# Optimization experiments

Measured on AMD Instinct MI355X. Metric: run time of the kernel, lower is better.

## Reference

```python
import jax, jax.numpy as jnp
import numpy as np

B, L, D = 32, 256, 1024
ALIGN = 1024
FF = 2048
NUM_CLASSES = 3


def setup_inputs() -> dict:
    key = jax.random.key(0)
    ks = jax.random.split(key, 10)
    u = lambda k, shape: jax.random.uniform(k, shape, jnp.float32, -1.0, 1.0)
    return {
        "premises": jax.random.normal(ks[0], (B, L, D), jnp.float32),
        "hypotheses": jax.random.normal(ks[1], (B, L, D), jnp.float32),
        "W_F": u(ks[2], (D, ALIGN)),
        "W_G": u(ks[3], (2 * D, FF)),
        "W1": u(ks[4], (2 * FF, FF)) * 0.02,
        "b1": jnp.zeros((FF,), jnp.float32),
        "W2": u(ks[5], (FF, FF)) * 0.02,
        "b2": jnp.zeros((FF,), jnp.float32),
        "W3": u(ks[6], (FF, NUM_CLASSES)) * 0.02,
        "b3": jnp.zeros((NUM_CLASSES,), jnp.float32),
    }


def reference(premises, hypotheses, W_F, W_G, W1, b1, W2, b2, W3, b3):
    # ---- align: tanh-projected cross attention ----
    F_p = jnp.tanh(jnp.einsum("bpd,da->bpa", premises, W_F))      # [B,Lp,A]
    F_h = jnp.tanh(jnp.einsum("bhd,da->bha", hypotheses, W_F))    # [B,Lh,A]
    eijs = jnp.einsum("bpa,bha->bph", F_p, F_h)                   # [B,Lp,Lh]
    attn = jax.nn.softmax(eijs, axis=-1)                          # tf.nn.softmax: last axis
    betas = jnp.einsum("bph,bhd->bpd", attn, hypotheses)          # [B,Lp,D]
    alphas = jnp.einsum("bph,bpd->bhd", attn, premises)           # [B,Lh,D]

    # ---- compare (dropout is identity: p_keep = 1.0 at eval) ----
    V1 = jnp.tanh(jnp.concatenate([premises, betas], axis=2) @ W_G)    # [B,Lp,FF]
    V2 = jnp.tanh(jnp.concatenate([hypotheses, alphas], axis=2) @ W_G) # [B,Lh,FF]

    # ---- aggregate: sum-pool over sequence, concat ----
    agg = jnp.concatenate([V1.sum(axis=1), V2.sum(axis=1)], axis=1)    # [B,2*FF]

    # ---- classifier MLP ----
    a1 = jnp.tanh(agg @ W1 + b1)
    a2 = jnp.tanh(a1 @ W2 + b2)
    logits = a2 @ W3 + b3                                              # [B,3]
    return logits
```

## Files before the change

### kernel.cpp

```cpp
#include <hip/hip_runtime.h>
#include <hip/hip_bf16.h>
#include <stdint.h>


typedef __attribute__((ext_vector_type(8))) short    short8_t;
typedef __attribute__((ext_vector_type(4))) float    float4_t;
typedef __attribute__((ext_vector_type(8))) _Float16 half8_t;
typedef __attribute__((ext_vector_type(4))) _Float16 half4_t;
typedef __attribute__((ext_vector_type(2))) _Float16 half2_t;

#define DEVI static __device__ __forceinline__

DEVI short f2bf(float f) {
  union { float f; unsigned u; } v; v.f = f;
  unsigned r = v.u + 0x7fffu + ((v.u >> 16) & 1u);
  return (short)(r >> 16);
}
DEVI float bf2f(short s) {
  union { unsigned u; float f; } v;
  v.u = ((unsigned)(unsigned short)s) << 16;
  return v.f;
}
DEVI void split2(float x, short& hi, short& lo) {
  hi = f2bf(x);
  lo = f2bf(x - bf2f(hi));
}
DEVI float fast_tanh(float x) {
  float e = __expf(2.0f * x);
  return 1.0f - 2.0f / (e + 1.0f);
}
DEVI void gload16(const void* g, void* l) {
  __builtin_amdgcn_global_load_lds(
      (const __attribute__((address_space(1))) void*)g,
      (__attribute__((address_space(3))) void*)l, 16, 0, 0);
}

template <int DO_TANH, int OUT_MODE>
__global__ __launch_bounds__(256) void gemm_nt_split(
    const short* __restrict__ Ah, const short* __restrict__ Al, int lda, long sA,
    const short* __restrict__ Bh, const short* __restrict__ Bl, int ldb, long sB,
    void* __restrict__ Ch, void* __restrict__ Cl, int ldc, long sC,
    int M, int K, int kslices)
{
  __shared__ __align__(16) short Ash[128 * 32];
  __shared__ __align__(16) short Asl[128 * 32];
  __shared__ __align__(16) short Bsh[128 * 32];
  __shared__ __align__(16) short Bsl[128 * 32];

  const int z  = blockIdx.z;
  const int zb = z / kslices;
  const int zk = z - zb * kslices;
  const int Ksub = K / kslices;
  const int kbeg = zk * Ksub, kend = kbeg + Ksub;

  Ah += (size_t)zb * sA;  Al += (size_t)zb * sA;
  Bh += (size_t)zb * sB;  Bl += (size_t)zb * sB;

  const int row0 = blockIdx.x * 128;
  const int col0 = blockIdx.y * 128;

  const int t    = threadIdx.x;
  const int lane = t & 63;
  const int wave = t >> 6;
  const int wr = wave >> 1, wc = wave & 1;
  const int m15 = lane & 15, q = lane >> 4;

  const int schk = ((t & 3) ^ ((t >> 3) & 3)) * 8;
  const short* pAh = Ah + (size_t)(row0 + (t >> 2)) * lda + kbeg + schk;
  const short* pAl = Al + (size_t)(row0 + (t >> 2)) * lda + kbeg + schk;
  const short* pBh = Bh + (size_t)(col0 + (t >> 2)) * ldb + kbeg + schk;
  const short* pBl = Bl + (size_t)(col0 + (t >> 2)) * ldb + kbeg + schk;
  const size_t a64 = (size_t)64 * lda, b64 = (size_t)64 * ldb;
  short* lAh = &Ash[wave * 512];
  short* lAl = &Asl[wave * 512];
  short* lBh = &Bsh[wave * 512];
  short* lBl = &Bsl[wave * 512];

  const int fs2 = (q ^ ((m15 >> 1) & 3)) * 8;

  float4_t acc[4][4];
#pragma unroll
  for (int i = 0; i < 4; ++i)
#pragma unroll
    for (int j = 0; j < 4; ++j) acc[i][j] = (float4_t)0.0f;

  for (int k0 = kbeg; k0 < kend; k0 += 32) {
    gload16(pAh, lAh);  gload16(pAh + a64, lAh + 2048);
    gload16(pAl, lAl);  gload16(pAl + a64, lAl + 2048);
    gload16(pBh, lBh);  gload16(pBh + b64, lBh + 2048);
    gload16(pBl, lBl);  gload16(pBl + b64, lBl + 2048);
    pAh += 32; pAl += 32; pBh += 32; pBl += 32;
    __syncthreads();

    short8_t ah[4], al[4];
#pragma unroll
    for (int i = 0; i < 4; ++i) {
      const int ra = (wr * 64 + i * 16 + m15) * 32 + fs2;
      ah[i] = *(const short8_t*)&Ash[ra];
      al[i] = *(const short8_t*)&Asl[ra];
    }
#pragma unroll
    for (int j = 0; j < 4; ++j) {
      const int rb = (wc * 64 + j * 16 + m15) * 32 + fs2;
      short8_t bh = *(const short8_t*)&Bsh[rb];
      short8_t bl = *(const short8_t*)&Bsl[rb];
#pragma unroll
      for (int i = 0; i < 4; ++i) {
        acc[i][j] = __builtin_amdgcn_mfma_f32_16x16x32_bf16(ah[i], bh, acc[i][j], 0, 0, 0);
        acc[i][j] = __builtin_amdgcn_mfma_f32_16x16x32_bf16(ah[i], bl, acc[i][j], 0, 0, 0);
        acc[i][j] = __builtin_amdgcn_mfma_f32_16x16x32_bf16(al[i], bh, acc[i][j], 0, 0, 0);
      }
    }
    __syncthreads();
  }

  short* Chs = (short*)Ch + (size_t)zb * sC;
  short* Cls = (short*)Cl + (size_t)zb * sC;
  float* Cf  = (float*)Ch + (size_t)zb * sC;
#pragma unroll
  for (int i = 0; i < 4; ++i) {
#pragma unroll
    for (int r = 0; r < 4; ++r) {
      int gm = row0 + wr * 64 + i * 16 + q * 4 + r;
      if (gm < M) {
#pragma unroll
        for (int j = 0; j < 4; ++j) {
          int gn = col0 + wc * 64 + j * 16 + m15;
          float v = acc[i][j][r];
          if (DO_TANH) v = fast_tanh(v);
          if (OUT_MODE == 0) {
            atomicAdd(&Cf[(size_t)gm * ldc + gn], v);
          } else {
            short hi, lo; split2(v, hi, lo);
            Chs[(size_t)gm * ldc + gn] = hi;
            Cls[(size_t)gm * ldc + gn] = lo;
          }
        }
      }
    }
  }
}

__global__ __launch_bounds__(256) void gemm_f16(
    const _Float16* __restrict__ A, int lda, long sA,
    const _Float16* __restrict__ B, int ldb, long sB,
    _Float16* __restrict__ C, int ldc, long sC,
    int K, int bxor)
{
  __shared__ __align__(16) _Float16 As[2 * 128 * 32];
  __shared__ __align__(16) _Float16 Bs[2 * 128 * 32];

  const int z = blockIdx.z;
  A += (size_t)z * sA;
  B += (size_t)(z ^ bxor) * sB;

  const int row0 = blockIdx.x * 128;
  const int col0 = blockIdx.y * 128;
  const int t = threadIdx.x, lane = t & 63, wave = t >> 6;
  const int wr = wave >> 1, wc = wave & 1;
  const int m15 = lane & 15, q = lane >> 4;

  const int srow = wave * 32 + (lane >> 2);
  const int cg   = ((lane & 3) ^ ((lane >> 3) & 3)) * 8;
  const _Float16* gA0 = A + (size_t)(row0 + srow) * lda + cg;
  const _Float16* gA1 = gA0 + (size_t)16 * lda;
  const _Float16* gB0 = B + (size_t)(col0 + srow) * ldb + cg;
  const _Float16* gB1 = gB0 + (size_t)16 * ldb;
  const _Float16* gA0b = gA0 + 32;
  const _Float16* gA1b = gA1 + 32;
  const _Float16* gB0b = gB0 + 32;
  const _Float16* gB1b = gB1 + 32;
  _Float16* lA0  = &As[(wave * 32) * 32];
  _Float16* lA1  = &As[(wave * 32 + 16) * 32];
  _Float16* lB0  = &Bs[(wave * 32) * 32];
  _Float16* lB1  = &Bs[(wave * 32 + 16) * 32];
  _Float16* lA0b = lA0 + 4096;
  _Float16* lA1b = lA1 + 4096;
  _Float16* lB0b = lB0 + 4096;
  _Float16* lB1b = lB1 + 4096;

  const int fs = (q ^ ((m15 >> 1) & 3)) * 8;
  int aoff[4], boff[4];
#pragma unroll
  for (int i = 0; i < 4; ++i) {
    aoff[i] = (wr * 64 + i * 16 + m15) * 32 + fs;
    boff[i] = (wc * 64 + i * 16 + m15) * 32 + fs;
  }

  float4_t acc[4][4];
#pragma unroll
  for (int i = 0; i < 4; ++i)
#pragma unroll
    for (int j = 0; j < 4; ++j) acc[i][j] = (float4_t)0.0f;

  for (int k0 = 0; k0 < K; k0 += 64) {
    gload16(gA0, lA0);  gload16(gA1, lA1);
    gload16(gB0, lB0);  gload16(gB1, lB1);
    gload16(gA0b, lA0b); gload16(gA1b, lA1b);
    gload16(gB0b, lB0b); gload16(gB1b, lB1b);
    gA0 += 64; gA1 += 64; gB0 += 64; gB1 += 64;
    gA0b += 64; gA1b += 64; gB0b += 64; gB1b += 64;
    __syncthreads();

#pragma unroll
    for (int h = 0; h < 2; ++h) {
      half8_t af[4], bfr[4];
#pragma unroll
      for (int i = 0; i < 4; ++i) af[i]  = *(const half8_t*)&As[h * 4096 + aoff[i]];
#pragma unroll
      for (int j = 0; j < 4; ++j) bfr[j] = *(const half8_t*)&Bs[h * 4096 + boff[j]];
#pragma unroll
      for (int i = 0; i < 4; ++i)
#pragma unroll
        for (int j = 0; j < 4; ++j)
          acc[i][j] = __builtin_amdgcn_mfma_f32_16x16x32_f16(af[i], bfr[j], acc[i][j], 0, 0, 0);
    }
    __syncthreads();
  }

  {
    _Float16* Cp = C + (size_t)z * sC;
#pragma unroll
    for (int i = 0; i < 4; ++i)
#pragma unroll
      for (int r = 0; r < 4; ++r) {
        int gm = row0 + wr * 64 + i * 16 + q * 4 + r;
#pragma unroll
        for (int j = 0; j < 4; ++j) {
          int gn = col0 + wc * 64 + j * 16 + m15;
          Cp[(size_t)gm * ldc + gn] = (_Float16)acc[i][j][r];
        }
      }
  }
}

__global__ __launch_bounds__(512, 2) void gemm_f16_sum8(
    const _Float16* __restrict__ A, int lda,
    const _Float16* __restrict__ B, int ldb,
    int K, float* __restrict__ agg)
{
  __shared__ __align__(16) _Float16 LDS[4][2 * 256 * 32];

  const int row0 = blockIdx.x * 256;
  const int col0 = blockIdx.y * 256;
  const int tid  = threadIdx.x;
  const int lane = tid & 63, wave = tid >> 6;
  const int wr = wave >> 2, wc = wave & 3;
  const int m15 = lane & 15, q = lane >> 4;
  const int nt = K / 32;

  const int srow = wave * 32 + (lane >> 2);
  const int cg   = ((lane & 3) ^ ((lane >> 3) & 3)) * 8;
  const _Float16* gA = A + (size_t)(row0 + srow) * lda + cg;
  const _Float16* gB = B + (size_t)(col0 + srow) * ldb + cg;

  auto stageA = [&](int t) {
    const _Float16* g = gA + t * 32;
    _Float16* l = &LDS[t & 3][wave * 1024];
    gload16(g, l);
    gload16(g + (size_t)16 * lda, l + 512);
  };
  auto stageB = [&](int t) {
    const _Float16* g = gB + t * 32;
    _Float16* l = &LDS[t & 3][8192 + wave * 1024];
    gload16(g, l);
    gload16(g + (size_t)16 * ldb, l + 512);
  };

  const int xq = (q ^ ((m15 >> 1) & 3)) * 8;
  int aoff[8], boff[4];
#pragma unroll
  for (int i = 0; i < 8; ++i)
    aoff[i] = (wr * 128 + i * 16 + m15) * 32 + xq;
#pragma unroll
  for (int j = 0; j < 4; ++j)
    boff[j] = 8192 + (wc * 64 + j * 16 + m15) * 32 + xq;

  float4_t acc[8][4];
#pragma unroll
  for (int i = 0; i < 8; ++i)
#pragma unroll
    for (int j = 0; j < 4; ++j) acc[i][j] = (float4_t)0.0f;

  stageA(0); stageB(0);
  stageA(1); stageB(1);
  asm volatile("s_waitcnt vmcnt(4)");
  __builtin_amdgcn_s_barrier();

  for (int t = 0; t < nt; ++t) {
    const _Float16* buf = &LDS[t & 3][0];
    __builtin_amdgcn_sched_barrier(0);

    half8_t a0[4], a1[4], bb[4];
#pragma unroll
    for (int i = 0; i < 4; ++i) a0[i] = *(const half8_t*)&buf[aoff[i]];
#pragma unroll
    for (int j = 0; j < 4; ++j) bb[j] = *(const half8_t*)&buf[boff[j]];
#pragma unroll
    for (int i = 0; i < 4; ++i) a1[i] = *(const half8_t*)&buf[aoff[4 + i]];

    if (t + 2 < nt) { stageA(t + 2); stageB(t + 2); }

    __builtin_amdgcn_s_setprio(1);
#pragma unroll
    for (int i = 0; i < 4; ++i)
#pragma unroll
      for (int j = 0; j < 4; ++j)
        acc[i][j] = __builtin_amdgcn_mfma_f32_16x16x32_f16(a0[i], bb[j], acc[i][j], 0, 0, 0);
#pragma unroll
    for (int i = 0; i < 4; ++i)
#pragma unroll
      for (int j = 0; j < 4; ++j)
        acc[4 + i][j] = __builtin_amdgcn_mfma_f32_16x16x32_f16(a1[i], bb[j], acc[4 + i][j], 0, 0, 0);
    __builtin_amdgcn_s_setprio(0);

    __builtin_amdgcn_sched_barrier(0);
    if (t + 2 < nt) {
      asm volatile("s_waitcnt vmcnt(4)");
    } else if (t + 1 < nt) {
      asm volatile("s_waitcnt vmcnt(0)");
    }
    __builtin_amdgcn_s_barrier();
  }

  const int half_ = row0 >= 8192;
  const int b     = (row0 & 8191) >> 8;
#pragma unroll
  for (int j = 0; j < 4; ++j) {
    float s = 0.0f;
#pragma unroll
    for (int i = 0; i < 8; ++i)
#pragma unroll
      for (int r = 0; r < 4; ++r) s += fast_tanh(acc[i][j][r]);
    s += __shfl_xor(s, 16);
    s += __shfl_xor(s, 32);
    if (q == 0) {
      int col = col0 + wc * 64 + j * 16 + m15;
      atomicAdd(&agg[(size_t)b * 4096 + half_ * 2048 + col], s);
    }
  }
}

__global__ __launch_bounds__(256) void transpose_split(
    const float* __restrict__ in, short* __restrict__ oh, short* __restrict__ ol,
    int R, int C)
{
  __shared__ float tile[32][33];
  const int tx = threadIdx.x & 31, ty = threadIdx.x >> 5;
  const int c0 = blockIdx.x * 32, r0 = blockIdx.y * 32;
#pragma unroll
  for (int i = 0; i < 4; ++i) {
    int r = ty + i * 8;
    tile[r][tx] = in[(size_t)(r0 + r) * C + c0 + tx];
  }
  __syncthreads();
#pragma unroll
  for (int i = 0; i < 4; ++i) {
    int cc = ty + i * 8;
    float v = tile[tx][cc];
    short hi, lo; split2(v, hi, lo);
    size_t o = (size_t)(c0 + cc) * R + r0 + tx;
    oh[o] = hi;
    ol[o] = lo;
  }
}

__global__ __launch_bounds__(256) void transpose_f16(
    const float* __restrict__ in, _Float16* __restrict__ out, int R, int C)
{
  __shared__ float tile[32][33];
  const int tx = threadIdx.x & 31, ty = threadIdx.x >> 5;
  const int c0 = blockIdx.x * 32, r0 = blockIdx.y * 32;
#pragma unroll
  for (int i = 0; i < 4; ++i) {
    int r = ty + i * 8;
    tile[r][tx] = in[(size_t)(r0 + r) * C + c0 + tx];
  }
  __syncthreads();
#pragma unroll
  for (int i = 0; i < 4; ++i) {
    int cc = ty + i * 8;
    out[(size_t)(c0 + cc) * R + r0 + tx] = (_Float16)tile[tx][cc];
  }
}

__global__ __launch_bounds__(256) void transpose_b2b(
    const short* __restrict__ in, short* __restrict__ out,
    int R, int C, long sIn, long sOut)
{
  __shared__ short tile[32][33];
  in  += (size_t)blockIdx.z * sIn;
  out += (size_t)blockIdx.z * sOut;
  const int tx = threadIdx.x & 31, ty = threadIdx.x >> 5;
  const int c0 = blockIdx.x * 32, r0 = blockIdx.y * 32;
#pragma unroll
  for (int i = 0; i < 4; ++i) {
    int r = ty + i * 8;
    tile[r][tx] = in[(size_t)(r0 + r) * C + c0 + tx];
  }
  __syncthreads();
#pragma unroll
  for (int i = 0; i < 4; ++i) {
    int cc = ty + i * 8;
    out[(size_t)(c0 + cc) * R + r0 + tx] = tile[tx][cc];
  }
}

__global__ __launch_bounds__(256) void conv_in_t(
    const float* __restrict__ P, const float* __restrict__ Hh,
    short* __restrict__ oh, short* __restrict__ ol,
    _Float16* __restrict__ cat, _Float16* __restrict__ phbt)
{
  __shared__ __align__(16) float tile[64][68];
  const int zb   = blockIdx.z;
  const int half = zb >> 5, b = zb & 31;
  const float* in = (half ? Hh : P) + (size_t)b * 256 * 1024;
  const int c0 = blockIdx.x * 64;
  const int r0 = blockIdx.y * 64;
  const int t  = threadIdx.x;
  const int rl = t >> 4;
  const int c4 = (t & 15) * 4;
  const size_t rowbase = (size_t)half * 8192 + (size_t)b * 256;
#pragma unroll
  for (int i = 0; i < 4; ++i) {
    int r = rl + i * 16;
    float4 v = *(const float4*)&in[(size_t)(r0 + r) * 1024 + c0 + c4];
    *(float4*)&tile[r][c4] = v;
    short4 h, l;
    split2(v.x, h.x, l.x); split2(v.y, h.y, l.y);
    split2(v.z, h.z, l.z); split2(v.w, h.w, l.w);
    size_t o = (rowbase + r0 + r) * 1024 + c0 + c4;
    *(short4*)&oh[o] = h;
    *(short4*)&ol[o] = l;
    half4_t c16;
    c16.x = (_Float16)v.x; c16.y = (_Float16)v.y;
    c16.z = (_Float16)v.z; c16.w = (_Float16)v.w;
    *(half4_t*)&cat[(rowbase + r0 + r) * 2048 + c0 + c4] = c16;
  }
  __syncthreads();
  _Float16* op = phbt + (size_t)zb * 1024 * 256;
  const int tx = t & 31;
  const int w  = t >> 5;
#pragma unroll
  for (int i = 0; i < 8; ++i) {
    int cc = w + i * 8;
    half2_t p;
    p.x = (_Float16)tile[tx * 2][cc];
    p.y = (_Float16)tile[tx * 2 + 1][cc];
    *(half2_t*)&op[(size_t)(c0 + cc) * 256 + r0 + tx * 2] = p;
  }
}

__global__ __launch_bounds__(256) void zero_f32(float* __restrict__ p, int n)
{
  int i = blockIdx.x * 256 + threadIdx.x;
  if (i < n) p[i] = 0.0f;
}

__global__ __launch_bounds__(256) void softmax_rows(
    const float* __restrict__ e, _Float16* __restrict__ attn)
{
  const int row  = blockIdx.x * 4 + (threadIdx.x >> 6);
  const int lane = threadIdx.x & 63;
  const float4 v = *(const float4*)&e[(size_t)row * 256 + lane * 4];
  float m = fmaxf(fmaxf(v.x, v.y), fmaxf(v.z, v.w));
#pragma unroll
  for (int off = 32; off; off >>= 1) m = fmaxf(m, __shfl_xor(m, off));
  float e0 = __expf(v.x - m), e1 = __expf(v.y - m);
  float e2 = __expf(v.z - m), e3 = __expf(v.w - m);
  float s = e0 + e1 + e2 + e3;
#pragma unroll
  for (int off = 32; off; off >>= 1) s += __shfl_xor(s, off);
  float inv = 1.0f / s;
  half4_t o;
  o.x = (_Float16)(e0 * inv); o.y = (_Float16)(e1 * inv);
  o.z = (_Float16)(e2 * inv); o.w = (_Float16)(e3 * inv);
  *(half4_t*)&attn[(size_t)row * 256 + lane * 4] = o;
}

__global__ __launch_bounds__(256) void skinny_gemm(
    const float* __restrict__ A, const float* __restrict__ B,
    float* __restrict__ out, int N, int K)
{
  __shared__ float Asl[256][33];
  const int n0 = blockIdx.x * 64;
  const int k0 = blockIdx.y * 256;
  const int t  = threadIdx.x;
#pragma unroll
  for (int j = 0; j < 32; ++j) {
    Asl[t][j] = A[(size_t)j * K + k0 + t];
  }
  __syncthreads();
  const int l = t & 63, w = t >> 6;
  const int n = n0 + l;
  float acc[8] = {0.f, 0.f, 0.f, 0.f, 0.f, 0.f, 0.f, 0.f};
  const float* Bp = B + (size_t)k0 * N + n;
#pragma unroll 4
  for (int k = 0; k < 256; ++k) {
    float bv = Bp[(size_t)k * N];
#pragma unroll
    for (int m = 0; m < 8; ++m)
      acc[m] += Asl[k][w * 8 + m] * bv;
  }
#pragma unroll
  for (int m = 0; m < 8; ++m)
    atomicAdd(&out[(size_t)(w * 8 + m) * N + n], acc[m]);
}

__global__ __launch_bounds__(256) void bias_tanh_f32(
    const float* __restrict__ c, const float* __restrict__ bias,
    float* __restrict__ o, int n)
{
  int i = blockIdx.x * 256 + threadIdx.x;
  if (i < n) o[i] = fast_tanh(c[i] + bias[i & 2047]);
}

__global__ __launch_bounds__(256) void logits2(
    const float* __restrict__ c2f, const float* __restrict__ b2,
    const float* __restrict__ W3, const float* __restrict__ b3,
    float* __restrict__ out)
{
  const int b = blockIdx.x, t = threadIdx.x;
  float p0 = 0.f, p1 = 0.f, p2 = 0.f;
  for (int k = t; k < 2048; k += 256) {
    float a = fast_tanh(c2f[b * 2048 + k] + b2[k]);
    p0 += a * W3[k * 3 + 0];
    p1 += a * W3[k * 3 + 1];
    p2 += a * W3[k * 3 + 2];
  }
#pragma unroll
  for (int off = 32; off; off >>= 1) {
    p0 += __shfl_xor(p0, off);
    p1 += __shfl_xor(p1, off);
    p2 += __shfl_xor(p2, off);
  }
  __shared__ float red[4][3];
  if ((t & 63) == 0) {
    red[t >> 6][0] = p0; red[t >> 6][1] = p1; red[t >> 6][2] = p2;
  }
  __syncthreads();
  if (t < 3) out[b * 3 + t] = b3[t] + red[0][t] + red[1][t] + red[2][t] + red[3][t];
}

extern "C" void kernel_launch(void* const* d_in, const int* in_sizes, int n_in,
                              void* d_out, int out_size, void* d_ws, size_t ws_size,
                              hipStream_t stream) {
  (void)in_sizes; (void)n_in; (void)out_size; (void)ws_size;
  const float* P   = (const float*)d_in[0];
  const float* H   = (const float*)d_in[1];
  const float* W_F = (const float*)d_in[2];
  const float* W_G = (const float*)d_in[3];
  const float* W1  = (const float*)d_in[4];
  const float* b1  = (const float*)d_in[5];
  const float* W2  = (const float*)d_in[6];
  const float* b2  = (const float*)d_in[7];
  const float* W3  = (const float*)d_in[8];
  const float* b3  = (const float*)d_in[9];
  float* out = (float*)d_out;

  char* wsp = (char*)d_ws;
  auto alloc = [&](size_t bytes) {
    char* p = wsp;
    wsp += (bytes + 255) & ~(size_t)255;
    return p;
  };
  short*    Pp_h  = (short*)alloc(16384ull * 1024 * 2);
  short*    Pp_l  = (short*)alloc(16384ull * 1024 * 2);
  _Float16* Cat16 = (_Float16*)alloc(16384ull * 2048 * 2);
  short*    Fbuf  = (short*)alloc(32ull * 1024 * 1024 * 2);
  _Float16* PHbT  = (_Float16*)alloc(64ull * 1024 * 256 * 2);
  short*    WFT_h = (short*)alloc(1024ull * 1024 * 2);
  short*    WFT_l = (short*)alloc(1024ull * 1024 * 2);
  _Float16* WGT16 = (_Float16*)alloc(2048ull * 2048 * 2);
  float*    eijs  = (float*)alloc(32ull * 256 * 256 * 4);
  _Float16* attn  = (_Float16*)alloc(32ull * 256 * 256 * 2);
  _Float16* attnT = (_Float16*)alloc(32ull * 256 * 256 * 2);
  float*    agg   = (float*)alloc(32ull * 4096 * 4);
  float*    c1f   = (float*)alloc(32ull * 2048 * 4);
  float*    c2f   = (float*)alloc(32ull * 2048 * 4);
  float*    a1f   = (float*)alloc(32ull * 2048 * 4);

  short* F_h = Fbuf;
  short* F_l = Fbuf + 16384ull * 1024;

  conv_in_t<<<dim3(16, 4, 64), 256, 0, stream>>>(P, H, Pp_h, Pp_l, Cat16, PHbT);
  transpose_split<<<dim3(32, 32, 1), 256, 0, stream>>>(W_F, WFT_h, WFT_l, 1024, 1024);
  transpose_f16<<<dim3(64, 64, 1), 256, 0, stream>>>(W_G, WGT16, 2048, 2048);

  gemm_nt_split<1, 1><<<dim3(128, 8, 1), 256, 0, stream>>>(
      Pp_h, Pp_l, 1024, 0, WFT_h, WFT_l, 1024, 0,
      F_h, F_l, 1024, 0, 16384, 1024, 1);

  zero_f32<<<8192, 256, 0, stream>>>(eijs, 32 * 256 * 256);
  gemm_nt_split<0, 0><<<dim3(2, 2, 128), 256, 0, stream>>>(
      F_h, F_l, 1024, 256 * 1024,
      F_h + 8192ull * 1024, F_l + 8192ull * 1024, 1024, 256 * 1024,
      eijs, nullptr, 256, 65536, 256, 1024, 4);

  softmax_rows<<<2048, 256, 0, stream>>>(eijs, attn);
  transpose_b2b<<<dim3(8, 8, 32), 256, 0, stream>>>(
      (const short*)attn, (short*)attnT, 256, 256, 65536, 65536);

  gemm_f16<<<dim3(2, 8, 64), 256, 0, stream>>>(
      attn, 256, 65536, PHbT, 256, 1024 * 256,
      Cat16 + 1024, 2048, 256 * 2048, 256, 32);

  zero_f32<<<512, 256, 0, stream>>>(agg, 32 * 4096);
  gemm_f16_sum8<<<dim3(64, 8, 1), 512, 0, stream>>>(
      Cat16, 2048, WGT16, 2048, 2048, agg);

  zero_f32<<<256, 256, 0, stream>>>(c1f, 32 * 2048);
  skinny_gemm<<<dim3(32, 16), 256, 0, stream>>>(agg, W1, c1f, 2048, 4096);
  bias_tanh_f32<<<256, 256, 0, stream>>>(c1f, b1, a1f, 32 * 2048);
  zero_f32<<<256, 256, 0, stream>>>(c2f, 32 * 2048);
  skinny_gemm<<<dim3(32, 8), 256, 0, stream>>>(a1f, W2, c2f, 2048, 2048);
  logits2<<<32, 256, 0, stream>>>(c2f, b2, W3, b3, out);
}
```

Baseline: 595.9 us.

## Replace split-K atomics with partial buffers and fuse zeroing and weight transposes

Split-K GEMMs (eijs and both classifier skinny GEMMs) now write per-slice partials into reused scratch buffers instead of atomically adding into zeroed outputs. The consumers (softmax, bias_tanh, logits) sum the slices themselves. This removes the zero_f32 launches and the atomic traffic. The two weight transposes are merged into one launch, and the agg zeroing moves into conv_in_t, cutting kernel launch count in exchange for extra partial-buffer reads.

```diff
diff --git a/kernel.cpp b/kernel.cpp
--- a/kernel.cpp
+++ b/kernel.cpp
@@ -49,8 +49,8 @@
 
   const int z  = blockIdx.z;
   const int zb = z / kslices;
+  const int Ksub = K / kslices;
   const int zk = z - zb * kslices;
-  const int Ksub = K / kslices;
   const int kbeg = zk * Ksub, kend = kbeg + Ksub;
 
   Ah += (size_t)zb * sA;  Al += (size_t)zb * sA;
@@ -116,7 +116,7 @@
 
   short* Chs = (short*)Ch + (size_t)zb * sC;
   short* Cls = (short*)Cl + (size_t)zb * sC;
-  float* Cf  = (float*)Ch + (size_t)zb * sC;
+  float* Cf  = (float*)Ch + (size_t)(OUT_MODE == 2 ? z : zb) * sC;
 #pragma unroll
   for (int i = 0; i < 4; ++i) {
 #pragma unroll
@@ -128,8 +128,8 @@
           int gn = col0 + wc * 64 + j * 16 + m15;
           float v = acc[i][j][r];
           if (DO_TANH) v = fast_tanh(v);
-          if (OUT_MODE == 0) {
-            atomicAdd(&Cf[(size_t)gm * ldc + gn], v);
+          if (OUT_MODE == 2) {
+            Cf[(size_t)gm * ldc + gn] = v;
           } else {
             short hi, lo; split2(v, hi, lo);
             Chs[(size_t)gm * ldc + gn] = hi;
@@ -341,46 +341,44 @@
   }
 }
 
-__global__ __launch_bounds__(256) void transpose_split(
-    const float* __restrict__ in, short* __restrict__ oh, short* __restrict__ ol,
-    int R, int C)
+__global__ __launch_bounds__(256) void transpose_w(
+    const float* __restrict__ WF, short* __restrict__ oh, short* __restrict__ ol,
+    const float* __restrict__ WG, _Float16* __restrict__ og)
 {
   __shared__ float tile[32][33];
+  const int id = blockIdx.x;
   const int tx = threadIdx.x & 31, ty = threadIdx.x >> 5;
-  const int c0 = blockIdx.x * 32, r0 = blockIdx.y * 32;
-#pragma unroll
-  for (int i = 0; i < 4; ++i) {
-    int r = ty + i * 8;
-    tile[r][tx] = in[(size_t)(r0 + r) * C + c0 + tx];
-  }
-  __syncthreads();
-#pragma unroll
-  for (int i = 0; i < 4; ++i) {
-    int cc = ty + i * 8;
-    float v = tile[tx][cc];
-    short hi, lo; split2(v, hi, lo);
-    size_t o = (size_t)(c0 + cc) * R + r0 + tx;
-    oh[o] = hi;
-    ol[o] = lo;
-  }
-}
-
-__global__ __launch_bounds__(256) void transpose_f16(
-    const float* __restrict__ in, _Float16* __restrict__ out, int R, int C)
-{
-  __shared__ float tile[32][33];
-  const int tx = threadIdx.x & 31, ty = threadIdx.x >> 5;
-  const int c0 = blockIdx.x * 32, r0 = blockIdx.y * 32;
-#pragma unroll
-  for (int i = 0; i < 4; ++i) {
-    int r = ty + i * 8;
-    tile[r][tx] = in[(size_t)(r0 + r) * C + c0 + tx];
-  }
-  __syncthreads();
-#pragma unroll
-  for (int i = 0; i < 4; ++i) {
-    int cc = ty + i * 8;
-    out[(size_t)(c0 + cc) * R + r0 + tx] = (_Float16)tile[tx][cc];
+  if (id < 1024) {
+    const int c0 = (id & 31) * 32, r0 = (id >> 5) * 32;
+#pragma unroll
+    for (int i = 0; i < 4; ++i) {
+      int r = ty + i * 8;
+      tile[r][tx] = WF[(size_t)(r0 + r) * 1024 + c0 + tx];
+    }
+    __syncthreads();
+#pragma unroll
+    for (int i = 0; i < 4; ++i) {
+      int cc = ty + i * 8;
+      float v = tile[tx][cc];
+      short hi, lo; split2(v, hi, lo);
+      size_t o = (size_t)(c0 + cc) * 1024 + r0 + tx;
+      oh[o] = hi;
+      ol[o] = lo;
+    }
+  } else {
+    const int t2 = id - 1024;
+    const int c0 = (t2 & 63) * 32, r0 = (t2 >> 6) * 32;
+#pragma unroll
+    for (int i = 0; i < 4; ++i) {
+      int r = ty + i * 8;
+      tile[r][tx] = WG[(size_t)(r0 + r) * 2048 + c0 + tx];
+    }
+    __syncthreads();
+#pragma unroll
+    for (int i = 0; i < 4; ++i) {
+      int cc = ty + i * 8;
+      og[(size_t)(c0 + cc) * 2048 + r0 + tx] = (_Float16)tile[tx][cc];
+    }
   }
 }
 
@@ -409,11 +407,17 @@
 __global__ __launch_bounds__(256) void conv_in_t(
     const float* __restrict__ P, const float* __restrict__ Hh,
     short* __restrict__ oh, short* __restrict__ ol,
-    _Float16* __restrict__ cat, _Float16* __restrict__ phbt)
+    _Float16* __restrict__ cat, _Float16* __restrict__ phbt,
+    float* __restrict__ agg)
 {
   __shared__ __align__(16) float tile[64][68];
   const int zb   = blockIdx.z;
   const int half = zb >> 5, b = zb & 31;
+  const int bid = (zb * 4 + blockIdx.y) * 16 + blockIdx.x;
+  if (bid < 128) {
+    float4_t zz = (float4_t)0.0f;
+    *(float4_t*)&agg[(size_t)bid * 1024 + threadIdx.x * 4] = zz;
+  }
   const float* in = (half ? Hh : P) + (size_t)b * 256 * 1024;
   const int c0 = blockIdx.x * 64;
   const int r0 = blockIdx.y * 64;
@@ -451,18 +455,22 @@
   }
 }
 
-__global__ __launch_bounds__(256) void zero_f32(float* __restrict__ p, int n)
-{
-  int i = blockIdx.x * 256 + threadIdx.x;
-  if (i < n) p[i] = 0.0f;
-}
-
 __global__ __launch_bounds__(256) void softmax_rows(
     const float* __restrict__ e, _Float16* __restrict__ attn)
 {
   const int row  = blockIdx.x * 4 + (threadIdx.x >> 6);
   const int lane = threadIdx.x & 63;
-  const float4 v = *(const float4*)&e[(size_t)row * 256 + lane * 4];
+  const size_t base = ((size_t)(row >> 8) * 4) * 65536
+                    + (size_t)(row & 255) * 256 + lane * 4;
+  const float4 v0 = *(const float4*)&e[base];
+  const float4 v1 = *(const float4*)&e[base + 65536];
+  const float4 v2 = *(const float4*)&e[base + 2 * 65536];
+  const float4 v3 = *(const float4*)&e[base + 3 * 65536];
+  float4 v;
+  v.x = (v0.x + v1.x) + (v2.x + v3.x);
+  v.y = (v0.y + v1.y) + (v2.y + v3.y);
+  v.z = (v0.z + v1.z) + (v2.z + v3.z);
+  v.w = (v0.w + v1.w) + (v2.w + v3.w);
   float m = fmaxf(fmaxf(v.x, v.y), fmaxf(v.z, v.w));
 #pragma unroll
   for (int off = 32; off; off >>= 1) m = fmaxf(m, __shfl_xor(m, off));
@@ -480,7 +488,7 @@
 
 __global__ __launch_bounds__(256) void skinny_gemm(
     const float* __restrict__ A, const float* __restrict__ B,
-    float* __restrict__ out, int N, int K)
+    float* __restrict__ outp, int N, int K)
 {
   __shared__ float Asl[256][33];
   const int n0 = blockIdx.x * 64;
@@ -502,28 +510,36 @@
     for (int m = 0; m < 8; ++m)
       acc[m] += Asl[k][w * 8 + m] * bv;
   }
+  float* o = outp + (size_t)blockIdx.y * 32 * N;
 #pragma unroll
   for (int m = 0; m < 8; ++m)
-    atomicAdd(&out[(size_t)(w * 8 + m) * N + n], acc[m]);
-}
-
-__global__ __launch_bounds__(256) void bias_tanh_f32(
-    const float* __restrict__ c, const float* __restrict__ bias,
-    float* __restrict__ o, int n)
+    o[(size_t)(w * 8 + m) * N + n] = acc[m];
+}
+
+__global__ __launch_bounds__(256) void bias_sum_tanh(
+    const float* __restrict__ parts, int nslice,
+    const float* __restrict__ bias, float* __restrict__ o, int n)
 {
   int i = blockIdx.x * 256 + threadIdx.x;
-  if (i < n) o[i] = fast_tanh(c[i] + bias[i & 2047]);
+  if (i < n) {
+    float s = 0.0f;
+    for (int sl = 0; sl < nslice; ++sl) s += parts[(size_t)sl * n + i];
+    o[i] = fast_tanh(s + bias[i & 2047]);
+  }
 }
 
 __global__ __launch_bounds__(256) void logits2(
-    const float* __restrict__ c2f, const float* __restrict__ b2,
+    const float* __restrict__ c2parts, const float* __restrict__ b2,
     const float* __restrict__ W3, const float* __restrict__ b3,
     float* __restrict__ out)
 {
   const int b = blockIdx.x, t = threadIdx.x;
   float p0 = 0.f, p1 = 0.f, p2 = 0.f;
   for (int k = t; k < 2048; k += 256) {
-    float a = fast_tanh(c2f[b * 2048 + k] + b2[k]);
+    float c = 0.0f;
+#pragma unroll
+    for (int sl = 0; sl < 8; ++sl) c += c2parts[(size_t)sl * 65536 + b * 2048 + k];
+    float a = fast_tanh(c + b2[k]);
     p0 += a * W3[k * 3 + 0];
     p1 += a * W3[k * 3 + 1];
     p2 += a * W3[k * 3 + 2];
@@ -572,32 +588,30 @@
   short*    WFT_h = (short*)alloc(1024ull * 1024 * 2);
   short*    WFT_l = (short*)alloc(1024ull * 1024 * 2);
   _Float16* WGT16 = (_Float16*)alloc(2048ull * 2048 * 2);
-  float*    eijs  = (float*)alloc(32ull * 256 * 256 * 4);
   _Float16* attn  = (_Float16*)alloc(32ull * 256 * 256 * 2);
   _Float16* attnT = (_Float16*)alloc(32ull * 256 * 256 * 2);
   float*    agg   = (float*)alloc(32ull * 4096 * 4);
-  float*    c1f   = (float*)alloc(32ull * 2048 * 4);
-  float*    c2f   = (float*)alloc(32ull * 2048 * 4);
   float*    a1f   = (float*)alloc(32ull * 2048 * 4);
 
   short* F_h = Fbuf;
   short* F_l = Fbuf + 16384ull * 1024;
-
-  conv_in_t<<<dim3(16, 4, 64), 256, 0, stream>>>(P, H, Pp_h, Pp_l, Cat16, PHbT);
-  transpose_split<<<dim3(32, 32, 1), 256, 0, stream>>>(W_F, WFT_h, WFT_l, 1024, 1024);
-  transpose_f16<<<dim3(64, 64, 1), 256, 0, stream>>>(W_G, WGT16, 2048, 2048);
+  float* eparts  = (float*)Pp_h;
+  float* c1parts = (float*)Pp_l;
+  float* c2parts = (float*)(Pp_l + 4ull * 1024 * 1024);
+
+  conv_in_t<<<dim3(16, 4, 64), 256, 0, stream>>>(P, H, Pp_h, Pp_l, Cat16, PHbT, agg);
+  transpose_w<<<5120, 256, 0, stream>>>(W_F, WFT_h, WFT_l, W_G, WGT16);
 
   gemm_nt_split<1, 1><<<dim3(128, 8, 1), 256, 0, stream>>>(
       Pp_h, Pp_l, 1024, 0, WFT_h, WFT_l, 1024, 0,
       F_h, F_l, 1024, 0, 16384, 1024, 1);
 
-  zero_f32<<<8192, 256, 0, stream>>>(eijs, 32 * 256 * 256);
-  gemm_nt_split<0, 0><<<dim3(2, 2, 128), 256, 0, stream>>>(
+  gemm_nt_split<0, 2><<<dim3(2, 2, 128), 256, 0, stream>>>(
       F_h, F_l, 1024, 256 * 1024,
       F_h + 8192ull * 1024, F_l + 8192ull * 1024, 1024, 256 * 1024,
-      eijs, nullptr, 256, 65536, 256, 1024, 4);
-
-  softmax_rows<<<2048, 256, 0, stream>>>(eijs, attn);
+      eparts, nullptr, 256, 65536, 256, 1024, 4);
+
+  softmax_rows<<<2048, 256, 0, stream>>>(eparts, attn);
   transpose_b2b<<<dim3(8, 8, 32), 256, 0, stream>>>(
       (const short*)attn, (short*)attnT, 256, 256, 65536, 65536);
 
@@ -605,14 +619,11 @@
       attn, 256, 65536, PHbT, 256, 1024 * 256,
       Cat16 + 1024, 2048, 256 * 2048, 256, 32);
 
-  zero_f32<<<512, 256, 0, stream>>>(agg, 32 * 4096);
   gemm_f16_sum8<<<dim3(64, 8, 1), 512, 0, stream>>>(
       Cat16, 2048, WGT16, 2048, 2048, agg);
 
-  zero_f32<<<256, 256, 0, stream>>>(c1f, 32 * 2048);
-  skinny_gemm<<<dim3(32, 16), 256, 0, stream>>>(agg, W1, c1f, 2048, 4096);
-  bias_tanh_f32<<<256, 256, 0, stream>>>(c1f, b1, a1f, 32 * 2048);
-  zero_f32<<<256, 256, 0, stream>>>(c2f, 32 * 2048);
-  skinny_gemm<<<dim3(32, 8), 256, 0, stream>>>(a1f, W2, c2f, 2048, 2048);
-  logits2<<<32, 256, 0, stream>>>(c2f, b2, W3, b3, out);
-}
+  skinny_gemm<<<dim3(32, 16), 256, 0, stream>>>(agg, W1, c1parts, 2048, 4096);
+  bias_sum_tanh<<<256, 256, 0, stream>>>(c1parts, 16, b1, a1f, 32 * 2048);
+  skinny_gemm<<<dim3(32, 8), 256, 0, stream>>>(a1f, W2, c2parts, 2048, 2048);
+  logits2<<<32, 256, 0, stream>>>(c2parts, b2, W3, b3, out);
+}
```

After: 560.4 us. -6.0%, faster.
